# Kernel tuning notes

Measured on AMD Instinct MI355X. Metric: run time of the kernel, lower is better.

Reference implementation:

```python
import jax, jax.numpy as jnp
import numpy as np

NY, NX = 1024, 2048
DX, DT, NU, UB = 1.0, 0.1, 0.01, 1.0
NITER = 5
NLEVEL = int(np.log2(NY)) + 1  # 11
DIAG = -8.0 / (3.0 * DX * DX)  # center coefficient of the Laplacian stencil wA


def _conv(x, w, stride=1):
    # single-channel 'VALID' cross-correlation, same semantics as torch Conv2d(padding=0)
    return jax.lax.conv_general_dilated(x, w, (stride, stride), 'VALID',
                                        dimension_numbers=('NCHW', 'OIHW', 'NCHW'))


def _bc_u(u):
    # inlet (left/top/bottom) = ub, zero-gradient outflow on the right
    uu = jnp.pad(u, ((0, 0), (0, 0), (1, 1), (1, 1)))
    uu = uu.at[:, :, :, 0].set(UB)
    uu = uu.at[:, :, :, -1].set(uu[:, :, :, -2])
    uu = uu.at[:, :, 0, :].set(UB)
    uu = uu.at[:, :, -1, :].set(UB)
    return uu


def _bc_v(v):
    # v = 0 on inlet/top/bottom (zero pad), zero-gradient outflow on the right
    vv = jnp.pad(v, ((0, 0), (0, 0), (1, 1), (1, 1)))
    vv = vv.at[:, :, :, -1].set(vv[:, :, :, -2])
    return vv


def _bc_p(p):
    # zero-gradient pressure except fixed p=0 at the outlet
    pp = jnp.pad(p, ((0, 0), (0, 0), (1, 1), (1, 1)))
    pp = pp.at[:, :, :, 0].set(pp[:, :, :, 1])
    pp = pp.at[:, :, :, -1].set(0.0)
    pp = pp.at[:, :, 0, :].set(pp[:, :, 1, :])
    pp = pp.at[:, :, -1, :].set(pp[:, :, -2, :])
    return pp


def _bc_cw(a):
    # homogeneous (zero) halo for the multigrid correction
    return jnp.pad(a, ((0, 0), (0, 0), (1, 1), (1, 1)))


def _prolong(a):
    return jnp.repeat(jnp.repeat(a, 2, axis=2), 2, axis=3)


def _f_cycle_mg(uu, vv, p, w_xadv, w_yadv, w_A, w_res):
    b = -(_conv(uu, w_xadv) + _conv(vv, w_yadv)) / DT
    for _ in range(NITER):
        r = _conv(_bc_p(p), w_A) - b
        r_s = [r]
        for _i in range(1, NLEVEL):
            r = _conv(r, w_res, stride=2)
            r_s.append(r)
        a = jnp.zeros((1, 1, 1, 1), dtype=p.dtype)
        for i in reversed(range(1, NLEVEL)):
            if i == NLEVEL - 1:
                a = r_s[i] / DIAG
            else:
                a = a - _conv(_bc_cw(a), w_A) / DIAG + r_s[i] / DIAG
            a = _prolong(a)
        p = p - a
        p = p - _conv(_bc_p(p), w_A) / DIAG + b / DIAG
    return p


def _forward(u, v, p, sigma, w_xadv, w_yadv, w_diff, w_A, w_res):
    uu, vv, pp = _bc_u(u), _bc_v(v), _bc_p(p)
    Grapx_p = _conv(pp, w_xadv) * DT
    Grapy_p = _conv(pp, w_yadv) * DT
    ADx_u, ADy_u = _conv(uu, w_xadv), _conv(uu, w_yadv)
    ADx_v, ADy_v = _conv(vv, w_xadv), _conv(vv, w_yadv)
    AD2_u, AD2_v = _conv(uu, w_diff), _conv(vv, w_diff)
    # predictor half-step
    bu = u + 0.5 * (NU * AD2_u * DT - u * ADx_u * DT - v * ADy_u * DT) - Grapx_p
    bv = v + 0.5 * (NU * AD2_v * DT - u * ADx_v * DT - v * ADy_v * DT) - Grapy_p
    damp = 1.0 / (1.0 + DT * sigma)  # solid body Brinkman penalty
    bu, bv = bu * damp, bv * damp
    buu, bvv = _bc_u(bu), _bc_v(bv)
    ADx_u, ADy_u = _conv(buu, w_xadv), _conv(buu, w_yadv)
    ADx_v, ADy_v = _conv(bvv, w_xadv), _conv(bvv, w_yadv)
    AD2_u, AD2_v = _conv(buu, w_diff), _conv(bvv, w_diff)
    # corrector step
    u = u + NU * AD2_u * DT - bu * ADx_u * DT - bv * ADy_u * DT - Grapx_p
    v = v + NU * AD2_v * DT - bu * ADx_v * DT - bv * ADy_v * DT - Grapy_p
    u, v = u * damp, v * damp
    uu, vv = _bc_u(u), _bc_v(v)
    # pressure solve via multigrid F-cycle + projection
    p = _f_cycle_mg(uu, vv, p, w_xadv, w_yadv, w_A, w_res)
    pp = _bc_p(p)
    u = u - _conv(pp, w_xadv) * DT
    v = v - _conv(pp, w_yadv) * DT
    u, v = u * damp, v * damp
    return jnp.concatenate([u, v, p], axis=1)  # (1, 3, NY, NX)


def setup_inputs() -> dict:
    key = jax.random.key(0)
    k1, k2, k3 = jax.random.split(key, 3)
    shp = (1, 1, NY, NX)
    u = jax.random.normal(k1, shp, jnp.float32) * 0.1 + UB
    v = jax.random.normal(k2, shp, jnp.float32) * 0.1
    p = jax.random.normal(k3, shp, jnp.float32) * 0.1
    # bluff-body mask: 1/timescale inside the rectangle (Block.create_solid_body_2D)
    cor_x, cor_y = NX // 4, NY // 2
    size_x, size_y = NX // 32, NY // 8
    sigma = jnp.zeros(shp, jnp.float32)
    sigma = sigma.at[0, 0, cor_y - size_y:cor_y + size_y,
                     cor_x - size_x:cor_x + size_x].set(1e8)
    # finite-difference stencils from get_weights_linear_2D(dx)
    w_diff = jnp.array([[1., 1., 1.], [1., -8., 1.], [1., 1., 1.]],
                       jnp.float32).reshape(1, 1, 3, 3) / (3.0 * DX * DX)
    w_xadv = jnp.array([[-1., 0., 1.], [-4., 0., 4.], [-1., 0., 1.]],
                       jnp.float32).reshape(1, 1, 3, 3) / (12.0 * DX)
    w_yadv = jnp.array([[-1., -4., -1.], [0., 0., 0.], [1., 4., 1.]],
                       jnp.float32).reshape(1, 1, 3, 3) / (12.0 * DX)
    w_A = w_diff
    w_res = jnp.full((1, 1, 2, 2), 0.25, jnp.float32)
    return {"u": u, "v": v, "p": p, "sigma": sigma, "w_xadv": w_xadv,
            "w_yadv": w_yadv, "w_diff": w_diff, "w_A": w_A, "w_res": w_res}


def reference(u, v, p, sigma, w_xadv, w_yadv, w_diff, w_A, w_res):
    return _forward(u, v, p, sigma, w_xadv, w_yadv, w_diff, w_A, w_res)
```

## Files before the change

### kernel.cpp

```cpp
#include <hip/hip_runtime.h>
#include <cstdint>

#define GNY 1024
#define GNX 2048
#define GNPTS (GNY * GNX)

namespace {
constexpr float DT = 0.1f;
constexpr float NUc = 0.01f;
constexpr float INV_DIAG = -0.375f;
}

__device__ __forceinline__ float bc_u_at(const float* __restrict__ f, int y, int x) {
    if (y < 0 || y >= GNY || x < 0) return 1.0f;
    if (x >= GNX) x = GNX - 1;
    return f[y * GNX + x];
}
__device__ __forceinline__ float bc_v_at(const float* __restrict__ f, int y, int x) {
    if (y < 0 || y >= GNY || x < 0) return 0.0f;
    if (x >= GNX) x = GNX - 1;
    return f[y * GNX + x];
}
__device__ __forceinline__ float bc_p_at(const float* __restrict__ f, int y, int x) {
    if (x >= GNX) return 0.0f;
    if (x < 0) x = 0;
    y = min(max(y, 0), GNY - 1);
    return f[y * GNX + x];
}

__device__ __forceinline__ float conv_x3(const float m[3][3]) {
    return ((m[0][2] - m[0][0]) + 4.0f * (m[1][2] - m[1][0]) + (m[2][2] - m[2][0])) * (1.0f / 12.0f);
}
__device__ __forceinline__ float conv_y3(const float m[3][3]) {
    return ((m[2][0] - m[0][0]) + 4.0f * (m[2][1] - m[0][1]) + (m[2][2] - m[0][2])) * (1.0f / 12.0f);
}
__device__ __forceinline__ float conv_d3(const float m[3][3]) {
    return (m[0][0] + m[0][1] + m[0][2] + m[1][0] + m[1][2] + m[2][0] + m[2][1] + m[2][2]
            - 8.0f * m[1][1]) * (1.0f / 3.0f);
}

template <typename PG>
__device__ __forceinline__ float up_val(PG pget, float rval, int H, int W, int y, int x) {
    float m[3][3];
#pragma unroll
    for (int dy = 0; dy < 3; ++dy)
#pragma unroll
        for (int dx = 0; dx < 3; ++dx) {
            int yy = y + dy - 1, xx = x + dx - 1;
            m[dy][dx] = (yy >= 0 && yy < H && xx >= 0 && xx < W) ? pget(yy >> 1, xx >> 1) : 0.0f;
        }
    float conv = (m[0][0] + m[0][1] + m[0][2] + m[1][0] + m[1][2]
                  + m[2][0] + m[2][1] + m[2][2] - 8.0f * m[1][1]) * (1.0f / 3.0f);
    return m[1][1] - conv * INV_DIAG + rval * INV_DIAG;
}

__global__ __launch_bounds__(256) void k_front(
        const float* __restrict__ u, const float* __restrict__ v,
        const float* __restrict__ p, const float* __restrict__ sigma,
        float* __restrict__ u2g, float* __restrict__ v2g, float* __restrict__ bg,
        float* __restrict__ r1, float* __restrict__ r2, float* __restrict__ r3,
        float* __restrict__ r4, float* __restrict__ r5) {
    __shared__ float sBu[36 * 37], sBv[36 * 37];
    __shared__ float sU2[34 * 35], sV2[34 * 35];
    __shared__ float s0[32 * 33];
    __shared__ float s1[16 * 17];
    __shared__ float s2[8 * 9];
    __shared__ float s3[4 * 5];
    __shared__ float s4[2 * 3];

    int t = threadIdx.x;
    int bx = blockIdx.x, by = blockIdx.y;
    int y0 = by * 32, x0 = bx * 32;

    for (int i = t; i < 1296; i += 256) {
        int wy = i / 36, wx = i - wy * 36;
        int gy = y0 - 2 + wy, gx = x0 - 2 + wx;
        float bu_ = 0.0f, bv_ = 0.0f;
        if (gy >= 0 && gy < GNY && gx >= 0 && gx < GNX) {
            float un[3][3], vn[3][3], pn[3][3];
#pragma unroll
            for (int dy = 0; dy < 3; ++dy)
#pragma unroll
                for (int dx = 0; dx < 3; ++dx) {
                    int yy = gy + dy - 1, xx = gx + dx - 1;
                    un[dy][dx] = bc_u_at(u, yy, xx);
                    vn[dy][dx] = bc_v_at(v, yy, xx);
                    pn[dy][dx] = bc_p_at(p, yy, xx);
                }
            float gxp = conv_x3(pn) * DT, gyp = conv_y3(pn) * DT;
            float uc = un[1][1], vc = vn[1][1];
            float damp = 1.0f / (1.0f + DT * sigma[gy * GNX + gx]);
            bu_ = (uc + 0.5f * (NUc * conv_d3(un) * DT - uc * conv_x3(un) * DT - vc * conv_y3(un) * DT) - gxp) * damp;
            bv_ = (vc + 0.5f * (NUc * conv_d3(vn) * DT - uc * conv_x3(vn) * DT - vc * conv_y3(vn) * DT) - gyp) * damp;
        }
        sBu[wy * 37 + wx] = bu_;
        sBv[wy * 37 + wx] = bv_;
    }
    __syncthreads();

    for (int i = t; i < 1156; i += 256) {
        int wy = i / 34, wx = i - wy * 34;
        int gy = y0 - 1 + wy, gx = x0 - 1 + wx;
        float u2_ = 0.0f, v2_ = 0.0f;
        if (gy >= 0 && gy < GNY && gx >= 0 && gx < GNX) {
            float bun[3][3], bvn[3][3], pn[3][3];
#pragma unroll
            for (int dy = 0; dy < 3; ++dy)
#pragma unroll
                for (int dx = 0; dx < 3; ++dx) {
                    int yy = gy + dy - 1, xx = gx + dx - 1;
                    float buv, bvv;
                    if (yy < 0 || yy >= GNY || xx < 0) { buv = 1.0f; bvv = 0.0f; }
                    else {
                        int cx = (xx >= GNX) ? GNX - 1 : xx;
                        int li = (yy - (y0 - 2)) * 37 + (cx - (x0 - 2));
                        buv = sBu[li]; bvv = sBv[li];
                    }
                    bun[dy][dx] = buv; bvn[dy][dx] = bvv;
                    pn[dy][dx] = bc_p_at(p, yy, xx);
                }
            float gxp = conv_x3(pn) * DT, gyp = conv_y3(pn) * DT;
            float buc = bun[1][1], bvc = bvn[1][1];
            int idx = gy * GNX + gx;
            float damp = 1.0f / (1.0f + DT * sigma[idx]);
            u2_ = (u[idx] + NUc * conv_d3(bun) * DT - buc * conv_x3(bun) * DT - bvc * conv_y3(bun) * DT - gxp) * damp;
            v2_ = (v[idx] + NUc * conv_d3(bvn) * DT - buc * conv_x3(bvn) * DT - bvc * conv_y3(bvn) * DT - gyp) * damp;
            if (wy >= 1 && wy <= 32 && wx >= 1 && wx <= 32) {
                u2g[idx] = u2_;
                v2g[idx] = v2_;
            }
        }
        sU2[wy * 35 + wx] = u2_;
        sV2[wy * 35 + wx] = v2_;
    }
    __syncthreads();

    for (int i = t; i < 1024; i += 256) {
        int ty = i >> 5, tx = i & 31;
        int gy = y0 + ty, gx = x0 + tx;
        float un[3][3], vn[3][3], pn[3][3];
#pragma unroll
        for (int dy = 0; dy < 3; ++dy)
#pragma unroll
            for (int dx = 0; dx < 3; ++dx) {
                int yy = gy + dy - 1, xx = gx + dx - 1;
                float uv, vv;
                if (yy < 0 || yy >= GNY || xx < 0) { uv = 1.0f; vv = 0.0f; }
                else {
                    int cx = (xx >= GNX) ? GNX - 1 : xx;
                    int li = (yy - (y0 - 1)) * 35 + (cx - (x0 - 1));
                    uv = sU2[li]; vv = sV2[li];
                }
                un[dy][dx] = uv; vn[dy][dx] = vv;
                pn[dy][dx] = bc_p_at(p, yy, xx);
            }
        float b_ = -(conv_x3(un) + conv_y3(vn)) * (1.0f / DT);
        bg[gy * GNX + gx] = b_;
        s0[ty * 33 + tx] = conv_d3(pn) - b_;
    }
    __syncthreads();

    { int qy = t >> 4, qx = t & 15;
      float vv = 0.25f * (s0[(2*qy)*33 + 2*qx] + s0[(2*qy)*33 + 2*qx + 1]
                        + s0[(2*qy+1)*33 + 2*qx] + s0[(2*qy+1)*33 + 2*qx + 1]);
      s1[qy*17 + qx] = vv;
      r1[(by*16 + qy)*1024 + bx*16 + qx] = vv; }
    __syncthreads();
    if (t < 64) { int qy = t >> 3, qx = t & 7;
      float vv = 0.25f * (s1[(2*qy)*17 + 2*qx] + s1[(2*qy)*17 + 2*qx + 1]
                        + s1[(2*qy+1)*17 + 2*qx] + s1[(2*qy+1)*17 + 2*qx + 1]);
      s2[qy*9 + qx] = vv;
      r2[(by*8 + qy)*512 + bx*8 + qx] = vv; }
    __syncthreads();
    if (t < 16) { int qy = t >> 2, qx = t & 3;
      float vv = 0.25f * (s2[(2*qy)*9 + 2*qx] + s2[(2*qy)*9 + 2*qx + 1]
                        + s2[(2*qy+1)*9 + 2*qx] + s2[(2*qy+1)*9 + 2*qx + 1]);
      s3[qy*5 + qx] = vv;
      r3[(by*4 + qy)*256 + bx*4 + qx] = vv; }
    __syncthreads();
    if (t < 4) { int qy = t >> 1, qx = t & 1;
      float vv = 0.25f * (s3[(2*qy)*5 + 2*qx] + s3[(2*qy)*5 + 2*qx + 1]
                        + s3[(2*qy+1)*5 + 2*qx] + s3[(2*qy+1)*5 + 2*qx + 1]);
      s4[qy*3 + qx] = vv;
      r4[(by*2 + qy)*128 + bx*2 + qx] = vv; }
    __syncthreads();
    if (t == 0)
        r5[by*64 + bx] = 0.25f * (s4[0] + s4[1] + s4[3] + s4[4]);
}

__global__ __launch_bounds__(256) void k_mg(
        const float* __restrict__ p_src, const float* __restrict__ b,
        const float* __restrict__ r1, const float* __restrict__ r2,
        const float* __restrict__ r3, const float* __restrict__ r4,
        const float* __restrict__ r5,
        float* __restrict__ p_dst,
        float* __restrict__ o1, float* __restrict__ o2, float* __restrict__ o3,
        float* __restrict__ o4, float* __restrict__ o5,
        const float* __restrict__ sigma, float* __restrict__ u_io,
        float* __restrict__ v_io, int last) {
    __shared__ float scr[3948];
    __shared__ float w6v[9], w5v[9], w4v[16], w3v[36], w2v[100], w1v[324];
    float* s5  = scr;
    float* s6  = scr + 2048;
    float* s7  = scr + 2560;
    float* s8  = scr + 2688;
    float* s9  = scr + 2720;
    float* s10 = scr + 2728;
    float* a9  = scr + 2730;
    float* a8  = scr + 2738;
    float* a7  = scr + 2770;
    float* sPp = scr;
    float* sPn = scr + 1332;
    float* s0  = scr + 2522;
    float* s1  = scr + 3578;
    float* s2  = scr + 3850;
    float* s3  = scr + 3922;
    float* s4  = scr + 3942;

    int t = threadIdx.x;
    int bx = blockIdx.x, by = blockIdx.y;
    int y0 = by * 32, x0 = bx * 32;

    for (int i = t; i < 2048; i += 256) s5[i] = r5[i];
    __syncthreads();
    for (int i = t; i < 512; i += 256) {
        int y = i >> 5, x = i & 31;
        s6[i] = 0.25f * (s5[(2*y)*64 + 2*x] + s5[(2*y)*64 + 2*x + 1]
                       + s5[(2*y+1)*64 + 2*x] + s5[(2*y+1)*64 + 2*x + 1]);
    }
    __syncthreads();
    if (t < 128) { int y = t >> 4, x = t & 15;
        s7[t] = 0.25f * (s6[(2*y)*32 + 2*x] + s6[(2*y)*32 + 2*x + 1]
                       + s6[(2*y+1)*32 + 2*x] + s6[(2*y+1)*32 + 2*x + 1]); }
    __syncthreads();
    if (t < 32) { int y = t >> 3, x = t & 7;
        s8[t] = 0.25f * (s7[(2*y)*16 + 2*x] + s7[(2*y)*16 + 2*x + 1]
                       + s7[(2*y+1)*16 + 2*x] + s7[(2*y+1)*16 + 2*x + 1]); }
    __syncthreads();
    if (t < 8) { int y = t >> 2, x = t & 3;
        s9[t] = 0.25f * (s8[(2*y)*8 + 2*x] + s8[(2*y)*8 + 2*x + 1]
                       + s8[(2*y+1)*8 + 2*x] + s8[(2*y+1)*8 + 2*x + 1]); }
    __syncthreads();
    if (t < 2)
        s10[t] = 0.25f * (s9[2*t] + s9[2*t + 1] + s9[4 + 2*t] + s9[4 + 2*t + 1]);
    __syncthreads();
    if (t < 8) { int y = t >> 2, x = t & 3;
        a9[t] = up_val([&](int py, int px) { return s10[py*2 + px] * INV_DIAG; },
                       s9[t], 2, 4, y, x); }
    __syncthreads();
    if (t < 32) { int y = t >> 3, x = t & 7;
        a8[t] = up_val([&](int py, int px) { return a9[py*4 + px]; },
                       s8[t], 4, 8, y, x); }
    __syncthreads();
    if (t < 128) { int y = t >> 4, x = t & 15;
        a7[t] = up_val([&](int py, int px) { return a8[py*8 + px]; },
                       s7[t], 8, 16, y, x); }
    __syncthreads();

    int w6ylo = (by - 2) >> 1, w6xlo = (bx - 2) >> 1;
    int w5ylo = by - 1,        w5xlo = bx - 1;
    int w4ylo = 2*by - 1,      w4xlo = 2*bx - 1;
    int w3ylo = 4*by - 1,      w3xlo = 4*bx - 1;
    int w2ylo = 8*by - 1,      w2xlo = 8*bx - 1;
    int w1ylo = 16*by - 1,     w1xlo = 16*bx - 1;

    if (t < 9) { int gy = w6ylo + t/3, gx = w6xlo + t%3;
        w6v[t] = (gy >= 0 && gy < 16 && gx >= 0 && gx < 32)
            ? up_val([&](int py, int px) { return a7[py*16 + px]; },
                     s6[gy*32 + gx], 16, 32, gy, gx) : 0.0f; }
    __syncthreads();
    if (t < 9) { int gy = w5ylo + t/3, gx = w5xlo + t%3;
        w5v[t] = (gy >= 0 && gy < 32 && gx >= 0 && gx < 64)
            ? up_val([&](int py, int px) { return w6v[(py - w6ylo)*3 + (px - w6xlo)]; },
                     s5[gy*64 + gx], 32, 64, gy, gx) : 0.0f; }
    __syncthreads();
    if (t < 16) { int gy = w4ylo + t/4, gx = w4xlo + t%4;
        w4v[t] = (gy >= 0 && gy < 64 && gx >= 0 && gx < 128)
            ? up_val([&](int py, int px) { return w5v[(py - w5ylo)*3 + (px - w5xlo)]; },
                     r4[gy*128 + gx], 64, 128, gy, gx) : 0.0f; }
    __syncthreads();
    if (t < 36) { int gy = w3ylo + t/6, gx = w3xlo + t%6;
        w3v[t] = (gy >= 0 && gy < 128 && gx >= 0 && gx < 256)
            ? up_val([&](int py, int px) { return w4v[(py - w4ylo)*4 + (px - w4xlo)]; },
                     r3[gy*256 + gx], 128, 256, gy, gx) : 0.0f; }
    __syncthreads();
    if (t < 100) { int gy = w2ylo + t/10, gx = w2xlo + t%10;
        w2v[t] = (gy >= 0 && gy < 256 && gx >= 0 && gx < 512)
            ? up_val([&](int py, int px) { return w3v[(py - w3ylo)*6 + (px - w3xlo)]; },
                     r2[gy*512 + gx], 256, 512, gy, gx) : 0.0f; }
    __syncthreads();
    for (int i = t; i < 324; i += 256) { int gy = w1ylo + i/18, gx = w1xlo + i%18;
        w1v[i] = (gy >= 0 && gy < 512 && gx >= 0 && gx < 1024)
            ? up_val([&](int py, int px) { return w2v[(py - w2ylo)*10 + (px - w2xlo)]; },
                     r1[gy*1024 + gx], 512, 1024, gy, gx) : 0.0f; }
    __syncthreads();

    for (int i = t; i < 1296; i += 256) {
        int wy = i / 36, wx = i % 36;
        int gy = y0 - 2 + wy, gx = x0 - 2 + wx;
        float v = 0.0f;
        if (gy >= 0 && gy < GNY && gx >= 0 && gx < GNX)
            v = p_src[gy*GNX + gx] - w1v[((gy >> 1) - w1ylo)*18 + ((gx >> 1) - w1xlo)];
        sPp[wy*37 + wx] = v;
    }
    __syncthreads();
    for (int i = t; i < 1156; i += 256) {
        int wy = i / 34, wx = i % 34;
        int gy = y0 - 1 + wy, gx = x0 - 1 + wx;
        float v = 0.0f;
        if (gy >= 0 && gy < GNY && gx >= 0 && gx < GNX) {
            float m[3][3];
#pragma unroll
            for (int dy = 0; dy < 3; ++dy)
#pragma unroll
                for (int dx = 0; dx < 3; ++dx) {
                    int yy = gy + dy - 1, xx = gx + dx - 1;
                    float tv;
                    if (xx >= GNX) tv = 0.0f;
                    else {
                        int cx = xx < 0 ? 0 : xx;
                        int cy = min(max(yy, 0), GNY - 1);
                        tv = sPp[(cy - (y0 - 2))*37 + (cx - (x0 - 2))];
                    }
                    m[dy][dx] = tv;
                }
            float conv = (m[0][0] + m[0][1] + m[0][2] + m[1][0] + m[1][2]
                          + m[2][0] + m[2][1] + m[2][2] - 8.0f*m[1][1]) * (1.0f / 3.0f);
            v = m[1][1] - conv * INV_DIAG + b[gy*GNX + gx] * INV_DIAG;
        }
        sPn[wy*35 + wx] = v;
    }
    __syncthreads();
    for (int i = t; i < 1024; i += 256) {
        int ty = i >> 5, tx = i & 31;
        p_dst[(y0 + ty)*GNX + x0 + tx] = sPn[(ty + 1)*35 + (tx + 1)];
    }

    if (!last) {
        for (int i = t; i < 1024; i += 256) {
            int ty = i >> 5, tx = i & 31;
            int gy = y0 + ty, gx = x0 + tx;
            float m[3][3];
#pragma unroll
            for (int dy = 0; dy < 3; ++dy)
#pragma unroll
                for (int dx = 0; dx < 3; ++dx) {
                    int yy = gy + dy - 1, xx = gx + dx - 1;
                    float tv;
                    if (xx >= GNX) tv = 0.0f;
                    else {
                        int cx = xx < 0 ? 0 : xx;
                        int cy = min(max(yy, 0), GNY - 1);
                        tv = sPn[(cy - (y0 - 1))*35 + (cx - (x0 - 1))];
                    }
                    m[dy][dx] = tv;
                }
            s0[ty*33 + tx] = conv_d3(m) - b[gy*GNX + gx];
        }
        __syncthreads();
        { int qy = t >> 4, qx = t & 15;
          float v = 0.25f * (s0[(2*qy)*33 + 2*qx] + s0[(2*qy)*33 + 2*qx + 1]
                           + s0[(2*qy+1)*33 + 2*qx] + s0[(2*qy+1)*33 + 2*qx + 1]);
          s1[qy*17 + qx] = v;
          o1[(by*16 + qy)*1024 + bx*16 + qx] = v; }
        __syncthreads();
        if (t < 64) { int qy = t >> 3, qx = t & 7;
          float v = 0.25f * (s1[(2*qy)*17 + 2*qx] + s1[(2*qy)*17 + 2*qx + 1]
                           + s1[(2*qy+1)*17 + 2*qx] + s1[(2*qy+1)*17 + 2*qx + 1]);
          s2[qy*9 + qx] = v;
          o2[(by*8 + qy)*512 + bx*8 + qx] = v; }
        __syncthreads();
        if (t < 16) { int qy = t >> 2, qx = t & 3;
          float v = 0.25f * (s2[(2*qy)*9 + 2*qx] + s2[(2*qy)*9 + 2*qx + 1]
                           + s2[(2*qy+1)*9 + 2*qx] + s2[(2*qy+1)*9 + 2*qx + 1]);
          s3[qy*5 + qx] = v;
          o3[(by*4 + qy)*256 + bx*4 + qx] = v; }
        __syncthreads();
        if (t < 4) { int qy = t >> 1, qx = t & 1;
          float v = 0.25f * (s3[(2*qy)*5 + 2*qx] + s3[(2*qy)*5 + 2*qx + 1]
                           + s3[(2*qy+1)*5 + 2*qx] + s3[(2*qy+1)*5 + 2*qx + 1]);
          s4[qy*3 + qx] = v;
          o4[(by*2 + qy)*128 + bx*2 + qx] = v; }
        __syncthreads();
        if (t == 0)
            o5[by*64 + bx] = 0.25f * (s4[0] + s4[1] + s4[3] + s4[4]);
    } else {
        for (int i = t; i < 1024; i += 256) {
            int ty = i >> 5, tx = i & 31;
            int gy = y0 + ty, gx = x0 + tx;
            float m[3][3];
#pragma unroll
            for (int dy = 0; dy < 3; ++dy)
#pragma unroll
                for (int dx = 0; dx < 3; ++dx) {
                    int yy = gy + dy - 1, xx = gx + dx - 1;
                    float tv;
                    if (xx >= GNX) tv = 0.0f;
                    else {
                        int cx = xx < 0 ? 0 : xx;
                        int cy = min(max(yy, 0), GNY - 1);
                        tv = sPn[(cy - (y0 - 1))*35 + (cx - (x0 - 1))];
                    }
                    m[dy][dx] = tv;
                }
            int idx = gy*GNX + gx;
            float damp = 1.0f / (1.0f + DT * sigma[idx]);
            u_io[idx] = (u_io[idx] - conv_x3(m) * DT) * damp;
            v_io[idx] = (v_io[idx] - conv_y3(m) * DT) * damp;
        }
    }
}

extern "C" void kernel_launch(void* const* d_in, const int* in_sizes, int n_in,
                              void* d_out, int out_size, void* d_ws, size_t ws_size,
                              hipStream_t stream) {
    (void)in_sizes; (void)n_in; (void)out_size; (void)ws_size;
    const float* u_in  = (const float*)d_in[0];
    const float* v_in  = (const float*)d_in[1];
    const float* p_in  = (const float*)d_in[2];
    const float* sigma = (const float*)d_in[3];

    float* out_u = (float*)d_out;
    float* out_v = out_u + GNPTS;
    float* out_p = out_u + 2 * (size_t)GNPTS;

    float* ws   = (float*)d_ws;
    float* b    = ws;
    float* p_ws = b + (size_t)GNPTS;
    float* base = p_ws + (size_t)GNPTS;
    float* A_[5], * B_[5];
    size_t lsz[5] = {524288, 131072, 32768, 8192, 2048};
    float* cur = base;
    for (int l = 0; l < 5; ++l) { A_[l] = cur; cur += lsz[l]; }
    for (int l = 0; l < 5; ++l) { B_[l] = cur; cur += lsz[l]; }

    dim3 grdT(GNX / 32, GNY / 32), blkT(256);

    k_front<<<grdT, blkT, 0, stream>>>(u_in, v_in, p_in, sigma,
                                       out_u, out_v, b,
                                       A_[0], A_[1], A_[2], A_[3], A_[4]);

    const float* p_cur = p_in;
    float* p_bufs[2] = { out_p, p_ws };
    for (int it = 0; it < 5; ++it) {
        float** rp = (it % 2 == 0) ? A_ : B_;
        float** wp = (it % 2 == 0) ? B_ : A_;
        float* p_next = p_bufs[it % 2];
        int last = (it == 4) ? 1 : 0;
        k_mg<<<grdT, blkT, 0, stream>>>(p_cur, b,
                                        rp[0], rp[1], rp[2], rp[3], rp[4],
                                        p_next,
                                        wp[0], wp[1], wp[2], wp[3], wp[4],
                                        sigma, out_u, out_v, last);
        p_cur = p_next;
    }
}
```

Baseline: 240.3 us.

## Stage p/u/v halo tiles in shared memory and bake boundary conditions into halos

```diff
diff --git a/kernel.cpp b/kernel.cpp
--- a/kernel.cpp
+++ b/kernel.cpp
@@ -60,78 +60,134 @@
         float* __restrict__ u2g, float* __restrict__ v2g, float* __restrict__ bg,
         float* __restrict__ r1, float* __restrict__ r2, float* __restrict__ r3,
         float* __restrict__ r4, float* __restrict__ r5) {
-    __shared__ float sBu[36 * 37], sBv[36 * 37];
-    __shared__ float sU2[34 * 35], sV2[34 * 35];
-    __shared__ float s0[32 * 33];
-    __shared__ float s1[16 * 17];
-    __shared__ float s2[8 * 9];
-    __shared__ float s3[4 * 5];
-    __shared__ float s4[2 * 3];
+    __shared__ float scrF[8442];
+    float* sP    = scrF;
+    float* sU    = scrF + 1482;
+    float* sV    = scrF + 2964;
+    float* sU2   = scrF + 1482;
+    float* sV2   = scrF + 2672;
+    float* sBu   = scrF + 4446;
+    float* sBv   = scrF + 5778;
+    float* sDamp = scrF + 7110;
+    float* s0    = scrF + 4446;
+    float* s1    = scrF + 5502;
+    float* s2    = scrF + 5774;
+    float* s3    = scrF + 5846;
+    float* s4    = scrF + 5866;
 
     int t = threadIdx.x;
     int bx = blockIdx.x, by = blockIdx.y;
     int y0 = by * 32, x0 = bx * 32;
+    bool edge = !(bx >= 1 && bx <= 62 && by >= 1 && by <= 30);
+    bool rightcol = (bx == 63);
+
+    if (!edge) {
+        for (int i = t; i < 1444; i += 256) {
+            int wy = i / 38, wx = i - wy * 38;
+            int idx = (y0 - 3 + wy) * GNX + (x0 - 3 + wx);
+            sP[wy * 39 + wx] = p[idx];
+            sU[wy * 39 + wx] = u[idx];
+            sV[wy * 39 + wx] = v[idx];
+        }
+    } else {
+        for (int i = t; i < 1444; i += 256) {
+            int wy = i / 38, wx = i - wy * 38;
+            int gy = y0 - 3 + wy, gx = x0 - 3 + wx;
+            sP[wy * 39 + wx] = bc_p_at(p, gy, gx);
+            sU[wy * 39 + wx] = bc_u_at(u, gy, gx);
+            sV[wy * 39 + wx] = bc_v_at(v, gy, gx);
+        }
+    }
+    __syncthreads();
 
     for (int i = t; i < 1296; i += 256) {
-        int wy = i / 36, wx = i - wy * 36;
-        int gy = y0 - 2 + wy, gx = x0 - 2 + wx;
-        float bu_ = 0.0f, bv_ = 0.0f;
-        if (gy >= 0 && gy < GNY && gx >= 0 && gx < GNX) {
-            float un[3][3], vn[3][3], pn[3][3];
-#pragma unroll
-            for (int dy = 0; dy < 3; ++dy)
-#pragma unroll
-                for (int dx = 0; dx < 3; ++dx) {
-                    int yy = gy + dy - 1, xx = gx + dx - 1;
-                    un[dy][dx] = bc_u_at(u, yy, xx);
-                    vn[dy][dx] = bc_v_at(v, yy, xx);
-                    pn[dy][dx] = bc_p_at(p, yy, xx);
-                }
+        int ay = i / 36, ax = i - ay * 36;
+        int gy = y0 - 2 + ay, gx = x0 - 2 + ax;
+        float un[3][3], vn[3][3], pn[3][3];
+#pragma unroll
+        for (int dy = 0; dy < 3; ++dy)
+#pragma unroll
+            for (int dx = 0; dx < 3; ++dx) {
+                int li = (ay + dy) * 39 + ax + dx;
+                un[dy][dx] = sU[li]; vn[dy][dx] = sV[li]; pn[dy][dx] = sP[li];
+            }
+        float buv, bvv, dampv = 0.0f;
+        bool valid = !edge || (gy >= 0 && gy < GNY && gx >= 0 && gx < GNX);
+        if (valid) {
+            dampv = 1.0f / (1.0f + DT * sigma[gy * GNX + gx]);
             float gxp = conv_x3(pn) * DT, gyp = conv_y3(pn) * DT;
             float uc = un[1][1], vc = vn[1][1];
-            float damp = 1.0f / (1.0f + DT * sigma[gy * GNX + gx]);
-            bu_ = (uc + 0.5f * (NUc * conv_d3(un) * DT - uc * conv_x3(un) * DT - vc * conv_y3(un) * DT) - gxp) * damp;
-            bv_ = (vc + 0.5f * (NUc * conv_d3(vn) * DT - uc * conv_x3(vn) * DT - vc * conv_y3(vn) * DT) - gyp) * damp;
-        }
-        sBu[wy * 37 + wx] = bu_;
-        sBv[wy * 37 + wx] = bv_;
-    }
-    __syncthreads();
-
-    for (int i = t; i < 1156; i += 256) {
-        int wy = i / 34, wx = i - wy * 34;
-        int gy = y0 - 1 + wy, gx = x0 - 1 + wx;
-        float u2_ = 0.0f, v2_ = 0.0f;
-        if (gy >= 0 && gy < GNY && gx >= 0 && gx < GNX) {
-            float bun[3][3], bvn[3][3], pn[3][3];
-#pragma unroll
-            for (int dy = 0; dy < 3; ++dy)
-#pragma unroll
-                for (int dx = 0; dx < 3; ++dx) {
-                    int yy = gy + dy - 1, xx = gx + dx - 1;
-                    float buv, bvv;
-                    if (yy < 0 || yy >= GNY || xx < 0) { buv = 1.0f; bvv = 0.0f; }
-                    else {
-                        int cx = (xx >= GNX) ? GNX - 1 : xx;
-                        int li = (yy - (y0 - 2)) * 37 + (cx - (x0 - 2));
-                        buv = sBu[li]; bvv = sBv[li];
-                    }
-                    bun[dy][dx] = buv; bvn[dy][dx] = bvv;
-                    pn[dy][dx] = bc_p_at(p, yy, xx);
+            buv = (uc + 0.5f * (NUc * conv_d3(un) * DT - uc * conv_x3(un) * DT - vc * conv_y3(un) * DT) - gxp) * dampv;
+            bvv = (vc + 0.5f * (NUc * conv_d3(vn) * DT - uc * conv_x3(vn) * DT - vc * conv_y3(vn) * DT) - gyp) * dampv;
+        } else if (gy < 0 || gy >= GNY || gx < 0) {
+            buv = 1.0f; bvv = 0.0f;
+        } else {
+            buv = 0.0f; bvv = 0.0f;
+        }
+        sBu[ay * 37 + ax] = buv;
+        sBv[ay * 37 + ax] = bvv;
+        sDamp[ay * 37 + ax] = dampv;
+    }
+    __syncthreads();
+
+    float ucA[5], vcA[5];
+    {
+        int np = 0;
+        for (int i = t; i < 1156; i += 256, ++np) {
+            int cy = i / 34, cx = i - cy * 34;
+            int li = (cy + 2) * 39 + cx + 2;
+            ucA[np] = sU[li]; vcA[np] = sV[li];
+        }
+    }
+    __syncthreads();
+    {
+        int np = 0;
+        for (int i = t; i < 1156; i += 256, ++np) {
+            int cy = i / 34, cx = i - cy * 34;
+            int gy = y0 - 1 + cy, gx = x0 - 1 + cx;
+            float u2_ = 0.0f, v2_ = 0.0f;
+            bool valid = (gy >= 0 && gy < GNY && gx >= 0 && gx < GNX);
+            if (valid) {
+                float bun[3][3], bvn[3][3], pn[3][3];
+                if (!rightcol) {
+#pragma unroll
+                    for (int dy = 0; dy < 3; ++dy)
+#pragma unroll
+                        for (int dx = 0; dx < 3; ++dx) {
+                            int li = (cy + dy) * 37 + cx + dx;
+                            bun[dy][dx] = sBu[li]; bvn[dy][dx] = sBv[li];
+                            pn[dy][dx] = sP[(cy + dy + 1) * 39 + cx + dx + 1];
+                        }
+                } else {
+#pragma unroll
+                    for (int dy = 0; dy < 3; ++dy)
+#pragma unroll
+                        for (int dx = 0; dx < 3; ++dx) {
+                            int yy = gy + dy - 1, xx = gx + dx - 1;
+                            pn[dy][dx] = sP[(cy + dy + 1) * 39 + cx + dx + 1];
+                            if (yy < 0 || yy >= GNY || xx < 0) { bun[dy][dx] = 1.0f; bvn[dy][dx] = 0.0f; }
+                            else {
+                                int cxx = (xx >= GNX) ? GNX - 1 : xx;
+                                int li = (cy + dy) * 37 + (cxx - (x0 - 2));
+                                bun[dy][dx] = sBu[li]; bvn[dy][dx] = sBv[li];
+                            }
+                        }
                 }
-            float gxp = conv_x3(pn) * DT, gyp = conv_y3(pn) * DT;
-            float buc = bun[1][1], bvc = bvn[1][1];
-            int idx = gy * GNX + gx;
-            float damp = 1.0f / (1.0f + DT * sigma[idx]);
-            u2_ = (u[idx] + NUc * conv_d3(bun) * DT - buc * conv_x3(bun) * DT - bvc * conv_y3(bun) * DT - gxp) * damp;
-            v2_ = (v[idx] + NUc * conv_d3(bvn) * DT - buc * conv_x3(bvn) * DT - bvc * conv_y3(bvn) * DT - gyp) * damp;
-            if (wy >= 1 && wy <= 32 && wx >= 1 && wx <= 32) {
-                u2g[idx] = u2_;
-                v2g[idx] = v2_;
+                float gxp = conv_x3(pn) * DT, gyp = conv_y3(pn) * DT;
+                float dampv = sDamp[(cy + 1) * 37 + cx + 1];
+                float buc = bun[1][1], bvc = bvn[1][1];
+                u2_ = (ucA[np] + NUc * conv_d3(bun) * DT - buc * conv_x3(bun) * DT - bvc * conv_y3(bun) * DT - gxp) * dampv;
+                v2_ = (vcA[np] + NUc * conv_d3(bvn) * DT - buc * conv_x3(bvn) * DT - bvc * conv_y3(bvn) * DT - gyp) * dampv;
+                if (cy >= 1 && cy <= 32 && cx >= 1 && cx <= 32) {
+                    int idx = gy * GNX + gx;
+                    u2g[idx] = u2_; v2g[idx] = v2_;
+                }
+            } else if (gy < 0 || gy >= GNY || gx < 0) {
+                u2_ = 1.0f; v2_ = 0.0f;
             }
-        }
-        sU2[wy * 35 + wx] = u2_;
-        sV2[wy * 35 + wx] = v2_;
+            sU2[cy * 35 + cx] = u2_;
+            sV2[cy * 35 + cx] = v2_;
+        }
     }
     __syncthreads();
 
@@ -139,21 +195,30 @@
         int ty = i >> 5, tx = i & 31;
         int gy = y0 + ty, gx = x0 + tx;
         float un[3][3], vn[3][3], pn[3][3];
-#pragma unroll
-        for (int dy = 0; dy < 3; ++dy)
-#pragma unroll
-            for (int dx = 0; dx < 3; ++dx) {
-                int yy = gy + dy - 1, xx = gx + dx - 1;
-                float uv, vv;
-                if (yy < 0 || yy >= GNY || xx < 0) { uv = 1.0f; vv = 0.0f; }
-                else {
-                    int cx = (xx >= GNX) ? GNX - 1 : xx;
-                    int li = (yy - (y0 - 1)) * 35 + (cx - (x0 - 1));
-                    uv = sU2[li]; vv = sV2[li];
+        if (!rightcol) {
+#pragma unroll
+            for (int dy = 0; dy < 3; ++dy)
+#pragma unroll
+                for (int dx = 0; dx < 3; ++dx) {
+                    int li = (ty + dy) * 35 + tx + dx;
+                    un[dy][dx] = sU2[li]; vn[dy][dx] = sV2[li];
+                    pn[dy][dx] = sP[(ty + dy + 2) * 39 + tx + dx + 2];
                 }
-                un[dy][dx] = uv; vn[dy][dx] = vv;
-                pn[dy][dx] = bc_p_at(p, yy, xx);
-            }
+        } else {
+#pragma unroll
+            for (int dy = 0; dy < 3; ++dy)
+#pragma unroll
+                for (int dx = 0; dx < 3; ++dx) {
+                    int yy = gy + dy - 1, xx = gx + dx - 1;
+                    pn[dy][dx] = sP[(ty + dy + 2) * 39 + tx + dx + 2];
+                    if (yy < 0 || yy >= GNY || xx < 0) { un[dy][dx] = 1.0f; vn[dy][dx] = 0.0f; }
+                    else {
+                        int cxx = (xx >= GNX) ? GNX - 1 : xx;
+                        int li = (ty + dy) * 35 + (cxx - (x0 - 1));
+                        un[dy][dx] = sU2[li]; vn[dy][dx] = sV2[li];
+                    }
+                }
+        }
         float b_ = -(conv_x3(un) + conv_y3(vn)) * (1.0f / DT);
         bg[gy * GNX + gx] = b_;
         s0[ty * 33 + tx] = conv_d3(pn) - b_;
@@ -296,37 +361,34 @@
     __syncthreads();
 
     for (int i = t; i < 1296; i += 256) {
-        int wy = i / 36, wx = i % 36;
-        int gy = y0 - 2 + wy, gx = x0 - 2 + wx;
+        int wy = i / 36, wx = i - wy * 36;
+        int yy = y0 - 2 + wy, xx = x0 - 2 + wx;
         float v = 0.0f;
-        if (gy >= 0 && gy < GNY && gx >= 0 && gx < GNX)
-            v = p_src[gy*GNX + gx] - w1v[((gy >> 1) - w1ylo)*18 + ((gx >> 1) - w1xlo)];
+        if (xx < GNX) {
+            int cy = min(max(yy, 0), GNY - 1);
+            int cx = xx < 0 ? 0 : xx;
+            v = p_src[cy*GNX + cx] - w1v[((cy >> 1) - w1ylo)*18 + ((cx >> 1) - w1xlo)];
+        }
         sPp[wy*37 + wx] = v;
     }
     __syncthreads();
     for (int i = t; i < 1156; i += 256) {
-        int wy = i / 34, wx = i % 34;
-        int gy = y0 - 1 + wy, gx = x0 - 1 + wx;
+        int wy = i / 34, wx = i - wy * 34;
+        int yy = y0 - 1 + wy, xx = x0 - 1 + wx;
         float v = 0.0f;
-        if (gy >= 0 && gy < GNY && gx >= 0 && gx < GNX) {
+        if (xx < GNX) {
+            int cy = min(max(yy, 0), GNY - 1);
+            int cx = xx < 0 ? 0 : xx;
+            int rb = cy - y0 + 2, cb = cx - x0 + 2;
             float m[3][3];
 #pragma unroll
             for (int dy = 0; dy < 3; ++dy)
 #pragma unroll
-                for (int dx = 0; dx < 3; ++dx) {
-                    int yy = gy + dy - 1, xx = gx + dx - 1;
-                    float tv;
-                    if (xx >= GNX) tv = 0.0f;
-                    else {
-                        int cx = xx < 0 ? 0 : xx;
-                        int cy = min(max(yy, 0), GNY - 1);
-                        tv = sPp[(cy - (y0 - 2))*37 + (cx - (x0 - 2))];
-                    }
-                    m[dy][dx] = tv;
-                }
+                for (int dx = 0; dx < 3; ++dx)
+                    m[dy][dx] = sPp[(rb + dy - 1)*37 + (cb + dx - 1)];
             float conv = (m[0][0] + m[0][1] + m[0][2] + m[1][0] + m[1][2]
                           + m[2][0] + m[2][1] + m[2][2] - 8.0f*m[1][1]) * (1.0f / 3.0f);
-            v = m[1][1] - conv * INV_DIAG + b[gy*GNX + gx] * INV_DIAG;
+            v = m[1][1] - conv * INV_DIAG + b[cy*GNX + cx] * INV_DIAG;
         }
         sPn[wy*35 + wx] = v;
     }
@@ -339,23 +401,13 @@
     if (!last) {
         for (int i = t; i < 1024; i += 256) {
             int ty = i >> 5, tx = i & 31;
-            int gy = y0 + ty, gx = x0 + tx;
             float m[3][3];
 #pragma unroll
             for (int dy = 0; dy < 3; ++dy)
 #pragma unroll
-                for (int dx = 0; dx < 3; ++dx) {
-                    int yy = gy + dy - 1, xx = gx + dx - 1;
-                    float tv;
-                    if (xx >= GNX) tv = 0.0f;
-                    else {
-                        int cx = xx < 0 ? 0 : xx;
-                        int cy = min(max(yy, 0), GNY - 1);
-                        tv = sPn[(cy - (y0 - 1))*35 + (cx - (x0 - 1))];
-                    }
-                    m[dy][dx] = tv;
-                }
-            s0[ty*33 + tx] = conv_d3(m) - b[gy*GNX + gx];
+                for (int dx = 0; dx < 3; ++dx)
+                    m[dy][dx] = sPn[(ty + dy)*35 + (tx + dx)];
+            s0[ty*33 + tx] = conv_d3(m) - b[(y0 + ty)*GNX + x0 + tx];
         }
         __syncthreads();
         { int qy = t >> 4, qx = t & 15;
@@ -387,23 +439,13 @@
     } else {
         for (int i = t; i < 1024; i += 256) {
             int ty = i >> 5, tx = i & 31;
-            int gy = y0 + ty, gx = x0 + tx;
             float m[3][3];
 #pragma unroll
             for (int dy = 0; dy < 3; ++dy)
 #pragma unroll
-                for (int dx = 0; dx < 3; ++dx) {
-                    int yy = gy + dy - 1, xx = gx + dx - 1;
-                    float tv;
-                    if (xx >= GNX) tv = 0.0f;
-                    else {
-                        int cx = xx < 0 ? 0 : xx;
-                        int cy = min(max(yy, 0), GNY - 1);
-                        tv = sPn[(cy - (y0 - 1))*35 + (cx - (x0 - 1))];
-                    }
-                    m[dy][dx] = tv;
-                }
-            int idx = gy*GNX + gx;
+                for (int dx = 0; dx < 3; ++dx)
+                    m[dy][dx] = sPn[(ty + dy)*35 + (tx + dx)];
+            int idx = (y0 + ty)*GNX + x0 + tx;
             float damp = 1.0f / (1.0f + DT * sigma[idx]);
             u_io[idx] = (u_io[idx] - conv_x3(m) * DT) * damp;
             v_io[idx] = (v_io[idx] - conv_y3(m) * DT) * damp;
```

New measurement: 220.1 us. 8.4% less time.
